# Optimization experiments

Hardware: AMD Instinct MI355X
Metric: run time of the kernel (lower is better)

The kernel has to match this reference:

```python
import jax, jax.numpy as jnp
import numpy as np

N = 40000       # nodes
E = 400000      # directed edges (before self-loops)
F_IN = 50       # PPI num_features
HID = 64        # per-head hidden
H = 4           # heads
NCLS = 121      # PPI num_classes
NEG_SLOPE = 0.2


def gat_layer(x, src, dst, W, a_src, a_dst, W_res, b, concat):
    """PyG GATConv: per-edge attention, segment softmax over dst, scatter-add."""
    n = x.shape[0]
    h, c = a_src.shape
    feat = (x @ W).reshape(n, h, c)                       # [N,H,C]
    al_s = (feat * a_src[None]).sum(-1)                   # [N,H]
    al_d = (feat * a_dst[None]).sum(-1)                   # [N,H]
    e = jax.nn.leaky_relu(al_s[src] + al_d[dst], NEG_SLOPE)  # [E,H]
    m = jax.ops.segment_max(e, dst, num_segments=n)       # stable softmax max
    e = jnp.exp(e - m[dst])
    denom = jax.ops.segment_sum(e, dst, num_segments=n)
    w = e / (denom[dst] + 1e-16)                          # [E,H] attention
    msg = feat[src] * w[:, :, None]                       # [E,H,C]
    out = jax.ops.segment_sum(msg, dst, num_segments=n)   # [N,H,C]
    out = out.reshape(n, h * c) if concat else out.mean(axis=1)
    return out + x @ W_res + b                            # residual proj + bias


def setup_inputs() -> dict:
    key = jax.random.key(0)
    ks = jax.random.split(key, 18)
    g = lambda k, shape: jax.random.normal(k, shape, dtype=jnp.float32) * 0.1
    return {
        "x": jax.random.normal(ks[0], (N, F_IN), dtype=jnp.float32),
        "edge_index": jax.random.randint(ks[1], (2, E), 0, N, dtype=jnp.int32),
        "W1": g(ks[2], (F_IN, H * HID)), "a1s": g(ks[3], (H, HID)), "a1d": g(ks[4], (H, HID)),
        "Wr1": g(ks[5], (F_IN, H * HID)), "b1": jnp.zeros((H * HID,), jnp.float32),
        "W2": g(ks[6], (H * HID, H * HID)), "a2s": g(ks[7], (H, HID)), "a2d": g(ks[8], (H, HID)),
        "Wr2": g(ks[9], (H * HID, H * HID)), "b2": jnp.zeros((H * HID,), jnp.float32),
        "W3": g(ks[10], (H * HID, H * NCLS)), "a3s": g(ks[11], (H, NCLS)), "a3d": g(ks[12], (H, NCLS)),
        "Wr3": g(ks[13], (H * HID, NCLS)), "b3": jnp.zeros((NCLS,), jnp.float32),
    }


def reference(x, edge_index, W1, a1s, a1d, Wr1, b1, W2, a2s, a2d, Wr2, b2,
              W3, a3s, a3d, Wr3, b3):
    loop = jnp.arange(N, dtype=edge_index.dtype)          # add_self_loops=True
    src = jnp.concatenate([edge_index[0], loop])
    dst = jnp.concatenate([edge_index[1], loop])
    h = jax.nn.relu(gat_layer(x, src, dst, W1, a1s, a1d, Wr1, b1, True))
    h = jax.nn.relu(gat_layer(h, src, dst, W2, a2s, a2d, Wr2, b2, True))
    return gat_layer(h, src, dst, W3, a3s, a3d, Wr3, b3, False)
```

## Files before the change

kernel.cpp:

```cpp
#include <hip/hip_runtime.h>
#include <hip/hip_bf16.h>


#define NNODES 40000
#define MPAD   40064
#define NEDGES 400000
#define FIN    50
#define NHEAD  4
#define SCANB  157
#define N4     160000

typedef __attribute__((ext_vector_type(8))) short short8;
typedef __attribute__((ext_vector_type(4))) float float4v;
typedef __attribute__((ext_vector_type(2))) float float2v;
typedef __attribute__((ext_vector_type(4))) unsigned short ushort4v;
typedef __attribute__((ext_vector_type(8))) unsigned short ushort8v;
typedef __attribute__((ext_vector_type(4))) unsigned int uint4v;

__device__ inline unsigned short f2bf(float f) {
    union { float f; unsigned u; } v; v.f = f;
    unsigned r = v.u + 0x7fff + ((v.u >> 16) & 1);
    return (unsigned short)(r >> 16);
}
__device__ inline float bf2f(unsigned short u) {
    union { unsigned u; float f; } v; v.u = ((unsigned)u) << 16; return v.f;
}
__device__ inline float lrelu(float x) { return x >= 0.f ? x : 0.2f * x; }

__global__ void hist_kernel(const int* __restrict__ dst, int* __restrict__ counts, int E) {
    int i = blockIdx.x * blockDim.x + threadIdx.x;
    if (i < E) atomicAdd(&counts[dst[i]], 1);
}

__global__ __launch_bounds__(256) void scan_local(const int* __restrict__ counts,
                                                  int* __restrict__ offsets,
                                                  int* __restrict__ partials) {
    __shared__ int sh[256];
    int b = blockIdx.x, t = threadIdx.x, i = b * 256 + t;
    int v = (i < NNODES) ? counts[i] : 0;
    sh[t] = v;
    __syncthreads();
    #pragma unroll
    for (int off = 1; off < 256; off <<= 1) {
        int u = (t >= off) ? sh[t - off] : 0;
        __syncthreads();
        sh[t] += u;
        __syncthreads();
    }
    if (i < NNODES) offsets[i] = sh[t] - v;
    if (t == 255) partials[b] = sh[255];
}

__global__ __launch_bounds__(256) void scan_partials(int* __restrict__ partials,
                                                     int* __restrict__ pexcl) {
    __shared__ int sh[256];
    int t = threadIdx.x;
    int v = (t < SCANB) ? partials[t] : 0;
    sh[t] = v;
    __syncthreads();
    #pragma unroll
    for (int off = 1; off < 256; off <<= 1) {
        int u = (t >= off) ? sh[t - off] : 0;
        __syncthreads();
        sh[t] += u;
        __syncthreads();
    }
    pexcl[t] = sh[t] - v;
}

__global__ __launch_bounds__(256) void scan_carry(int* __restrict__ offsets,
                                                  const int* __restrict__ pexcl) {
    int b = blockIdx.x, i = b * 256 + threadIdx.x;
    if (i < NNODES) offsets[i] += pexcl[b];
}

__global__ void scatter_kernel(const int* __restrict__ src, const int* __restrict__ dst,
                               int* __restrict__ offsets,
                               int* __restrict__ csr_src, int* __restrict__ csr_dst, int E) {
    int i = blockIdx.x * blockDim.x + threadIdx.x;
    if (i < E) {
        int d = dst[i];
        int pos = atomicAdd(&offsets[d], 1);
        csr_src[pos] = src[i];
        csr_dst[pos] = d;
    }
}

__global__ void edge_p(const float* __restrict__ al4,
                       const int* __restrict__ csr_src, const int* __restrict__ csr_dst,
                       float* __restrict__ p4, int E) {
    int j = blockIdx.x * blockDim.x + threadIdx.x;
    if (j >= E) return;
    int s = csr_src[j], d = csr_dst[j];
    float4v a0 = *(const float4v*)&al4[s * 4];
    float4v a1 = *(const float4v*)&al4[2 * N4 + s * 4];
    float4v b0 = *(const float4v*)&al4[N4 + d * 4];
    float4v b1 = *(const float4v*)&al4[3 * N4 + d * 4];
    float4v p;
    p.x = __expf(lrelu(a0.x + a1.x + b0.x + b1.x));
    p.y = __expf(lrelu(a0.y + a1.y + b0.y + b1.y));
    p.z = __expf(lrelu(a0.z + a1.z + b0.z + b1.z));
    p.w = __expf(lrelu(a0.w + a1.w + b0.w + b1.w));
    *(float4v*)&p4[(size_t)j * 4] = p;
}

__global__ void convert_x(const float* __restrict__ x, short* __restrict__ xb) {
    int i = blockIdx.x * blockDim.x + threadIdx.x;
    if (i >= MPAD * 64) return;
    int r = i >> 6, k = i & 63;
    float v = (r < NNODES && k < FIN) ? x[r * FIN + k] : 0.f;
    xb[i] = f2bf(v);
}

__global__ void convert_pack1(const float* __restrict__ W1, const float* __restrict__ Wr1,
                              const float* __restrict__ W2, const float* __restrict__ Wr2,
                              short* __restrict__ wc1, short* __restrict__ wc2) {
    int i = blockIdx.x * blockDim.x + threadIdx.x;
    if (i < 32768) {
        const float* W = (i < 16384) ? W1 : Wr1;
        int j = i & 16383;
        int n = j >> 6, k = j & 63;
        wc1[i] = f2bf((k < FIN) ? W[k * 256 + n] : 0.f);
    } else if (i < 163840) {
        int j = (i - 32768) & 65535;
        const float* W = (i < 98304) ? W2 : Wr2;
        int n = j >> 8, k = j & 255;
        wc2[(i - 32768)] = f2bf(W[k * 256 + n]);
    }
}

__global__ void convert_pack2(const float* __restrict__ W3, const float* __restrict__ Wr3,
                              const float* __restrict__ a3s, const float* __restrict__ a3d,
                              short* __restrict__ wc3,
                              float* __restrict__ a3sp, float* __restrict__ a3dp) {
    int i = blockIdx.x * blockDim.x + threadIdx.x;
    if (i < 131072) {
        int j = i >> 8, k = i & 255;
        int h = j >> 7, c = j & 127;
        wc3[i] = f2bf((c < 121) ? W3[k * 484 + h * 121 + c] : 0.f);
    } else if (i < 163840) {
        int j = i - 131072;
        int n = j >> 8, k = j & 255;
        wc3[131072 + j] = f2bf((n < 121) ? Wr3[k * 121 + n] : 0.f);
    } else if (i < 164864) {
        int j = i - 163840;
        int which = j >> 9; int jj = j & 511;
        int h = jj >> 7, c = jj & 127;
        float v = (c < 121) ? (which ? a3d[h * 121 + c] : a3s[h * 121 + c]) : 0.f;
        (which ? a3dp : a3sp)[jj] = v;
    }
}

__global__ void convert_f8(const unsigned short* __restrict__ Fb, unsigned int* __restrict__ F8) {
    int i = blockIdx.x * blockDim.x + threadIdx.x;
    if (i >= NNODES * 128) return;
    ushort4v f = *(const ushort4v*)&Fb[(size_t)i * 4];
    int v = 0;
    v = __builtin_amdgcn_cvt_pk_fp8_f32(bf2f(f.x), bf2f(f.y), v, false);
    v = __builtin_amdgcn_cvt_pk_fp8_f32(bf2f(f.z), bf2f(f.w), v, true);
    F8[i] = (unsigned int)v;
}

template<int MODE>
__global__ __launch_bounds__(256) void mfma_gemm_fused(const short* __restrict__ A,
                                                       const short* __restrict__ Bt,
                                                       const float* __restrict__ bias,
                                                       const float* __restrict__ asv,
                                                       const float* __restrict__ adv,
                                                       unsigned short* __restrict__ Fb,
                                                       unsigned short* __restrict__ Rb,
                                                       float* __restrict__ out,
                                                       float* __restrict__ al4,
                                                       int Kp) {
    const int NW = MODE ? 512 : 256;
    __shared__ __align__(16) short As[4096];
    __shared__ __align__(16) unsigned short Cs[2][32][132];
    const int tid = threadIdx.x;
    const int l   = tid & 63;
    const int w   = tid >> 6;
    const int wm  = w >> 1, wn = w & 1;
    const int row0 = blockIdx.y * 128;
    const int col0 = blockIdx.x * 128;
    const int lrow = l & 15;
    const int lq   = l >> 4;
    const int sr = (tid >> 6) * 16 + (tid & 15);
    const int sk = ((tid >> 4) & 3) * 8;

    float4v acc[4][4] = {};

    for (int k0 = 0; k0 < Kp; k0 += 32) {
        short8 a0 = *(const short8*)&A[(size_t)(row0 + sr) * Kp + k0 + sk];
        short8 a1 = *(const short8*)&A[(size_t)(row0 + 64 + sr) * Kp + k0 + sk];
        short8 bfrag[4];
        #pragma unroll
        for (int ct = 0; ct < 4; ++ct) {
            int col = col0 + wn * 64 + ct * 16 + lrow;
            bfrag[ct] = *(const short8*)&Bt[(size_t)col * Kp + k0 + lq * 8];
        }
        __syncthreads();
        *(short8*)&As[tid * 8] = a0;
        *(short8*)&As[(tid + 256) * 8] = a1;
        __syncthreads();
        #pragma unroll
        for (int rt = 0; rt < 4; ++rt) {
            short8 afrag = *(const short8*)&As[(wm * 4 + rt) * 512 + l * 8];
            #pragma unroll
            for (int ct = 0; ct < 4; ++ct)
                acc[rt][ct] = __builtin_amdgcn_mfma_f32_16x16x32_bf16(afrag, bfrag[ct],
                                                                      acc[rt][ct], 0, 0, 0);
        }
    }

    const int colbase = col0 + wn * 64;
    const bool isW = colbase < NW;

    if (isW) {
        const int head = (colbase * NHEAD) / NW;
        const int half = MODE ? ((colbase >> 6) & 1) : 0;
        float* als_o = al4 + (half ? 2 * N4 : 0);
        float* ald_o = als_o + N4;
        float as_c[4], ad_c[4];
        #pragma unroll
        for (int ct = 0; ct < 4; ++ct) {
            int col = colbase + ct * 16 + lrow;
            as_c[ct] = asv[col];
            ad_c[ct] = adv[col];
        }
        #pragma unroll
        for (int rt = 0; rt < 4; ++rt) {
            #pragma unroll
            for (int i = 0; i < 4; ++i) {
                int r = row0 + wm * 64 + rt * 16 + lq * 4 + i;
                float fs = 0.f, fd = 0.f;
                #pragma unroll
                for (int ct = 0; ct < 4; ++ct) {
                    float v = acc[rt][ct][i];
                    fs += v * as_c[ct];
                    fd += v * ad_c[ct];
                }
                #pragma unroll
                for (int o2 = 8; o2; o2 >>= 1) {
                    fs += __shfl_xor(fs, o2, 16);
                    fd += __shfl_xor(fd, o2, 16);
                }
                if (lrow == 0 && r < NNODES) {
                    als_o[r * 4 + head] = fs;
                    ald_o[r * 4 + head] = fd;
                }
            }
        }
    }

    if (MODE == 1 && col0 >= 512) {
        #pragma unroll
        for (int ct = 0; ct < 4; ++ct) {
            int c = colbase + ct * 16 + lrow - 512;
            if (c >= 121) continue;
            float bv = bias[c];
            #pragma unroll
            for (int rt = 0; rt < 4; ++rt) {
                int rbase = row0 + wm * 64 + rt * 16 + lq * 4;
                #pragma unroll
                for (int i = 0; i < 4; ++i) {
                    int r = rbase + i;
                    if (r < NNODES) out[(size_t)r * 121 + c] = acc[rt][ct][i] + bv;
                }
            }
        }
        return;
    }

    const bool isRb = (MODE == 0) && (col0 >= 256);
    unsigned short* dest = isRb ? Rb : Fb;
    const int ldd = MODE ? 512 : 256;
    const int cold = isRb ? col0 - 256 : col0;
    float badd[4] = {0.f, 0.f, 0.f, 0.f};
    if (isRb) {
        #pragma unroll
        for (int ct = 0; ct < 4; ++ct)
            badd[ct] = bias[col0 - 256 + wn * 64 + ct * 16 + lrow];
    }

    const int rp = tid >> 2, g = rp >> 5, rr = rp & 31, q = tid & 3;
    #pragma unroll
    for (int p = 0; p < 2; ++p) {
        if (p) __syncthreads();
        #pragma unroll
        for (int rt2 = 0; rt2 < 2; ++rt2) {
            int rt = p * 2 + rt2;
            #pragma unroll
            for (int ct = 0; ct < 4; ++ct) {
                int cl = wn * 64 + ct * 16 + lrow;
                #pragma unroll
                for (int i = 0; i < 4; ++i) {
                    int lr = rt2 * 16 + lq * 4 + i;
                    Cs[wm][lr][cl] = f2bf(acc[rt][ct][i] + badd[ct]);
                }
            }
        }
        __syncthreads();
        int grow = row0 + g * 64 + p * 32 + rr;
        if (grow < NNODES) {
            #pragma unroll
            for (int k = 0; k < 4; ++k) {
                ushort8v v = *(const ushort8v*)&Cs[g][rr][q * 32 + 8 * k];
                *(ushort8v*)&dest[(size_t)grow * ldd + cold + q * 32 + 8 * k] = v;
            }
        }
    }
}

__global__ __launch_bounds__(256) void attn64_kernel(const unsigned short* __restrict__ featb,
                                                     const float* __restrict__ al4,
                                                     const int* __restrict__ offs,
                                                     const int* __restrict__ csr,
                                                     const float* __restrict__ p4,
                                                     const unsigned short* __restrict__ Rb,
                                                     unsigned short* __restrict__ outb) {
    int n = blockIdx.x * 4 + (threadIdx.x >> 6);
    int l = threadIdx.x & 63;
    int half = l >> 5, li = l & 31;
    int h = li >> 3;
    int beg = n ? offs[n - 1] : 0;
    int end = offs[n];

    float a[8] = {};
    float s = 0.f;
    #pragma unroll 4
    for (int j = beg + half; j < end; j += 2) {
        int sn = csr[j];
        float p = p4[(size_t)j * 4 + h];
        s += p;
        ushort8v f = *(const ushort8v*)&featb[(size_t)sn * 256 + 8 * li];
        #pragma unroll
        for (int i = 0; i < 8; ++i) a[i] += p * bf2f(f[i]);
    }
    s += __shfl_xor(s, 32, 64);
    #pragma unroll
    for (int i = 0; i < 8; ++i) a[i] += __shfl_xor(a[i], 32, 64);

    float lg = al4[n * 4 + h] + al4[2 * N4 + n * 4 + h]
             + al4[N4 + n * 4 + h] + al4[3 * N4 + n * 4 + h];
    float p0 = __expf(lrelu(lg));
    s += p0;
    {
        ushort8v f = *(const ushort8v*)&featb[(size_t)n * 256 + 8 * li];
        #pragma unroll
        for (int i = 0; i < 8; ++i) a[i] += p0 * bf2f(f[i]);
    }
    if (half == 0) {
        float inv = 1.f / s;
        ushort8v r = *(const ushort8v*)&Rb[(size_t)n * 256 + 8 * li];
        ushort8v o;
        #pragma unroll
        for (int i = 0; i < 8; ++i) o[i] = f2bf(fmaxf(bf2f(r[i]) + a[i] * inv, 0.f));
        *(ushort8v*)&outb[(size_t)n * 256 + 8 * li] = o;
    }
}

__global__ __launch_bounds__(256) void attn121_kernel(const unsigned int* __restrict__ F8,
                                                      const float* __restrict__ al4,
                                                      const int* __restrict__ offs,
                                                      const int* __restrict__ csr,
                                                      const float* __restrict__ p4,
                                                      float* __restrict__ out) {
    int n = blockIdx.x * 4 + (threadIdx.x >> 6);
    int l = threadIdx.x & 63;
    int half = l >> 5, li = l & 31;
    int h = li >> 3;
    int beg = n ? offs[n - 1] : 0;
    int end = offs[n];

    float a[16] = {};
    float s = 0.f;
    #pragma unroll 2
    for (int j = beg + half; j < end; j += 2) {
        int sn = csr[j];
        float p = p4[(size_t)j * 4 + h];
        s += p;
        uint4v u = *(const uint4v*)&F8[(size_t)sn * 128 + 4 * li];
        #pragma unroll
        for (int k = 0; k < 4; ++k) {
            float2v lo = __builtin_amdgcn_cvt_pk_f32_fp8(u[k], false);
            float2v hi = __builtin_amdgcn_cvt_pk_f32_fp8(u[k], true);
            a[4 * k + 0] += p * lo.x; a[4 * k + 1] += p * lo.y;
            a[4 * k + 2] += p * hi.x; a[4 * k + 3] += p * hi.y;
        }
    }
    s += __shfl_xor(s, 32, 64);
    #pragma unroll
    for (int i = 0; i < 16; ++i) a[i] += __shfl_xor(a[i], 32, 64);

    float lg = al4[n * 4 + h] + al4[2 * N4 + n * 4 + h]
             + al4[N4 + n * 4 + h] + al4[3 * N4 + n * 4 + h];
    float p0 = __expf(lrelu(lg));
    s += p0;
    {
        uint4v u = *(const uint4v*)&F8[(size_t)n * 128 + 4 * li];
        #pragma unroll
        for (int k = 0; k < 4; ++k) {
            float2v lo = __builtin_amdgcn_cvt_pk_f32_fp8(u[k], false);
            float2v hi = __builtin_amdgcn_cvt_pk_f32_fp8(u[k], true);
            a[4 * k + 0] += p0 * lo.x; a[4 * k + 1] += p0 * lo.y;
            a[4 * k + 2] += p0 * hi.x; a[4 * k + 3] += p0 * hi.y;
        }
    }
    float inv = 0.25f / s;
    #pragma unroll
    for (int i = 0; i < 16; ++i) {
        a[i] *= inv;
        a[i] += __shfl_xor(a[i], 8, 64);
        a[i] += __shfl_xor(a[i], 16, 64);
    }
    if (l < 8) {
        #pragma unroll
        for (int i = 0; i < 16; ++i) {
            int c = 16 * l + i;
            if (c < 121) out[(size_t)n * 121 + c] += a[i];
        }
    }
}

extern "C" void kernel_launch(void* const* d_in, const int* in_sizes, int n_in,
                              void* d_out, int out_size, void* d_ws, size_t ws_size,
                              hipStream_t stream) {
    const float* x   = (const float*)d_in[0];
    const int* ei    = (const int*)d_in[1];
    const float* W1  = (const float*)d_in[2];
    const float* a1s = (const float*)d_in[3];
    const float* a1d = (const float*)d_in[4];
    const float* Wr1 = (const float*)d_in[5];
    const float* b1  = (const float*)d_in[6];
    const float* W2  = (const float*)d_in[7];
    const float* a2s = (const float*)d_in[8];
    const float* a2d = (const float*)d_in[9];
    const float* Wr2 = (const float*)d_in[10];
    const float* b2  = (const float*)d_in[11];
    const float* W3  = (const float*)d_in[12];
    const float* a3s = (const float*)d_in[13];
    const float* a3d = (const float*)d_in[14];
    const float* Wr3 = (const float*)d_in[15];
    const float* b3  = (const float*)d_in[16];
    float* out = (float*)d_out;

    const int* e_src = ei;
    const int* e_dst = ei + NEDGES;

    char* ws = (char*)d_ws;
    size_t off = 0;
    auto carve = [&](size_t bytes) { void* p = ws + off; off += (bytes + 255) & ~255ull; return p; };
    unsigned short* Fb = (unsigned short*)carve((size_t)MPAD * 512 * 2);
    unsigned short* Rb = (unsigned short*)carve((size_t)MPAD * 256 * 2);
    unsigned short* Hb = (unsigned short*)carve((size_t)MPAD * 256 * 2);
    unsigned int* F8 = (unsigned int*)carve((size_t)NNODES * 128 * 4);
    short* xb   = (short*)carve((size_t)MPAD * 64 * 2);
    short* wc1  = (short*)carve((size_t)512 * 64 * 2);
    short* wc2  = (short*)carve((size_t)512 * 256 * 2);
    short* wc3  = (short*)carve((size_t)640 * 256 * 2);
    float* a3sp = (float*)carve(512 * 4);
    float* a3dp = (float*)carve(512 * 4);
    float* al4  = (float*)carve((size_t)4 * N4 * 4);
    float* p4   = (float*)carve((size_t)NEDGES * 4 * 4);
    int* csr_src = (int*)carve((size_t)NEDGES * 4);
    int* csr_dst = (int*)carve((size_t)NEDGES * 4);
    int* offsets = (int*)carve(((size_t)NNODES + 4) * 4);
    int* counts  = (int*)carve((size_t)NNODES * 4);
    int* partials = (int*)carve(256 * 4);
    int* pexcl    = (int*)carve(256 * 4);

    const int EB = (NEDGES + 255) / 256;
    dim3 blk(256);

    convert_x<<<(MPAD * 64 + 255) / 256, blk, 0, stream>>>(x, xb);
    convert_pack1<<<(163840 + 255) / 256, blk, 0, stream>>>(W1, Wr1, W2, Wr2, wc1, wc2);
    convert_pack2<<<(164864 + 255) / 256, blk, 0, stream>>>(W3, Wr3, a3s, a3d, wc3, a3sp, a3dp);

    hipMemsetAsync(al4 + 2 * N4, 0, (size_t)2 * N4 * 4, stream);

    hipMemsetAsync(counts, 0, NNODES * 4, stream);
    hist_kernel<<<EB, blk, 0, stream>>>(e_dst, counts, NEDGES);
    scan_local<<<SCANB, blk, 0, stream>>>(counts, offsets, partials);
    scan_partials<<<1, blk, 0, stream>>>(partials, pexcl);
    scan_carry<<<SCANB, blk, 0, stream>>>(offsets, pexcl);
    scatter_kernel<<<EB, blk, 0, stream>>>(e_src, e_dst, offsets, csr_src, csr_dst, NEDGES);

    mfma_gemm_fused<0><<<dim3(4, 313), blk, 0, stream>>>(xb, wc1, b1, a1s, a1d,
                                                         Fb, Rb, nullptr, al4, 64);
    edge_p<<<EB, blk, 0, stream>>>(al4, csr_src, csr_dst, p4, NEDGES);
    attn64_kernel<<<NNODES / 4, blk, 0, stream>>>(Fb, al4, offsets, csr_src, p4, Rb, Hb);

    mfma_gemm_fused<0><<<dim3(4, 313), blk, 0, stream>>>((short*)Hb, wc2, b2, a2s, a2d,
                                                         Fb, Rb, nullptr, al4, 256);
    edge_p<<<EB, blk, 0, stream>>>(al4, csr_src, csr_dst, p4, NEDGES);
    attn64_kernel<<<NNODES / 4, blk, 0, stream>>>(Fb, al4, offsets, csr_src, p4, Rb, Hb);

    mfma_gemm_fused<1><<<dim3(5, 313), blk, 0, stream>>>((short*)Hb, wc3, b3, a3sp, a3dp,
                                                         Fb, nullptr, out, al4, 256);
    convert_f8<<<(NNODES * 128 + 255) / 256, blk, 0, stream>>>(Fb, F8);
    edge_p<<<EB, blk, 0, stream>>>(al4, csr_src, csr_dst, p4, NEDGES);
    attn121_kernel<<<NNODES / 4, blk, 0, stream>>>(F8, al4, offsets, csr_src, p4, out);
}
```

Before: 458.3 us.

## Stage GEMM tiles via direct global-to-LDS loads with XCD-aware block remap

The fused MFMA GEMM now loads both A and B tiles straight into LDS with global_load_lds, using K-steps of 64 instead of per-lane register loads of B. It also remaps the flat workgroup index so consecutive tiles land on the same XCD for better L2 reuse, and stages the final-layer fp32 output through LDS so row writes coalesce. The aim is to cut redundant global B traffic and uncoalesced stores. In exchange LDS use grows to 32KB for A/B, which may lower occupancy, and the grid dimensions are hardcoded to 313 row blocks.

```diff
diff --git a/kernel.cpp b/kernel.cpp
--- a/kernel.cpp
+++ b/kernel.cpp
@@ -26,6 +26,12 @@
     union { unsigned u; float f; } v; v.u = ((unsigned)u) << 16; return v.f;
 }
 __device__ inline float lrelu(float x) { return x >= 0.f ? x : 0.2f * x; }
+
+typedef __attribute__((address_space(3))) unsigned int lds_u32;
+typedef __attribute__((address_space(1))) const unsigned int glb_u32;
+__device__ __forceinline__ void gl2lds16(const short* g, short* l) {
+    __builtin_amdgcn_global_load_lds((glb_u32*)g, (lds_u32*)l, 16, 0, 0);
+}
 
 __global__ void hist_kernel(const int* __restrict__ dst, int* __restrict__ counts, int E) {
     int i = blockIdx.x * blockDim.x + threadIdx.x;
@@ -172,42 +178,59 @@
                                                        float* __restrict__ out,
                                                        float* __restrict__ al4,
                                                        int Kp) {
-    const int NW = MODE ? 512 : 256;
-    __shared__ __align__(16) short As[4096];
+    const int NW  = MODE ? 512 : 256;
+    const int NCB = MODE ? 5 : 4;
+    __shared__ __align__(16) short AsBs[16384];
     __shared__ __align__(16) unsigned short Cs[2][32][132];
+    short* As = AsBs;
+    short* Bs = AsBs + 8192;
+
     const int tid = threadIdx.x;
     const int l   = tid & 63;
     const int w   = tid >> 6;
     const int wm  = w >> 1, wn = w & 1;
-    const int row0 = blockIdx.y * 128;
-    const int col0 = blockIdx.x * 128;
     const int lrow = l & 15;
     const int lq   = l >> 4;
-    const int sr = (tid >> 6) * 16 + (tid & 15);
-    const int sk = ((tid >> 4) & 3) * 8;
+
+    const int T = NCB * 313;
+    const int flat = blockIdx.y * NCB + blockIdx.x;
+    const int q8 = T >> 3, r8 = T & 7;
+    const int xcd = flat & 7, sidx = flat >> 3;
+    const int wg = (xcd < r8 ? xcd * (q8 + 1) : r8 * (q8 + 1) + (xcd - r8) * q8) + sidx;
+    const int row0 = (wg / NCB) * 128;
+    const int col0 = (wg % NCB) * 128;
 
     float4v acc[4][4] = {};
 
-    for (int k0 = 0; k0 < Kp; k0 += 32) {
-        short8 a0 = *(const short8*)&A[(size_t)(row0 + sr) * Kp + k0 + sk];
-        short8 a1 = *(const short8*)&A[(size_t)(row0 + 64 + sr) * Kp + k0 + sk];
-        short8 bfrag[4];
-        #pragma unroll
-        for (int ct = 0; ct < 4; ++ct) {
-            int col = col0 + wn * 64 + ct * 16 + lrow;
-            bfrag[ct] = *(const short8*)&Bt[(size_t)col * Kp + k0 + lq * 8];
+    const int lr_ld = tid >> 3;
+    const int lk_ld = (tid & 7) * 8;
+    const int nk = Kp >> 6;
+    for (int t = 0; t < nk; ++t) {
+        const int k0 = t << 6;
+        if (t) __syncthreads();
+        const size_t abase = (size_t)(row0 + lr_ld) * Kp + k0 + lk_ld;
+        const size_t bbase = (size_t)(col0 + lr_ld) * Kp + k0 + lk_ld;
+        #pragma unroll
+        for (int j = 0; j < 4; ++j) {
+            gl2lds16(&A[abase + (size_t)j * 32 * Kp],  &As[j * 2048 + tid * 8]);
+            gl2lds16(&Bt[bbase + (size_t)j * 32 * Kp], &Bs[j * 2048 + tid * 8]);
         }
         __syncthreads();
-        *(short8*)&As[tid * 8] = a0;
-        *(short8*)&As[(tid + 256) * 8] = a1;
-        __syncthreads();
-        #pragma unroll
-        for (int rt = 0; rt < 4; ++rt) {
-            short8 afrag = *(const short8*)&As[(wm * 4 + rt) * 512 + l * 8];
+        #pragma unroll
+        for (int ks = 0; ks < 2; ++ks) {
+            short8 aF[4], bF[4];
+            #pragma unroll
+            for (int rt = 0; rt < 4; ++rt)
+                aF[rt] = *(const short8*)&As[(wm * 64 + rt * 16 + lrow) * 64 + ks * 32 + lq * 8];
             #pragma unroll
             for (int ct = 0; ct < 4; ++ct)
-                acc[rt][ct] = __builtin_amdgcn_mfma_f32_16x16x32_bf16(afrag, bfrag[ct],
-                                                                      acc[rt][ct], 0, 0, 0);
+                bF[ct] = *(const short8*)&Bs[(wn * 64 + ct * 16 + lrow) * 64 + ks * 32 + lq * 8];
+            #pragma unroll
+            for (int rt = 0; rt < 4; ++rt)
+                #pragma unroll
+                for (int ct = 0; ct < 4; ++ct)
+                    acc[rt][ct] = __builtin_amdgcn_mfma_f32_16x16x32_bf16(aF[rt], bF[ct],
+                                                                          acc[rt][ct], 0, 0, 0);
         }
     }
 
@@ -252,19 +275,34 @@
     }
 
     if (MODE == 1 && col0 >= 512) {
-        #pragma unroll
-        for (int ct = 0; ct < 4; ++ct) {
-            int c = colbase + ct * 16 + lrow - 512;
-            if (c >= 121) continue;
-            float bv = bias[c];
-            #pragma unroll
-            for (int rt = 0; rt < 4; ++rt) {
-                int rbase = row0 + wm * 64 + rt * 16 + lq * 4;
+        float* Ls = (float*)AsBs;
+        #pragma unroll
+        for (int p = 0; p < 4; ++p) {
+            __syncthreads();
+            if (wm == (p >> 1)) {
+                const int rt0 = (p & 1) * 2;
                 #pragma unroll
-                for (int i = 0; i < 4; ++i) {
-                    int r = rbase + i;
-                    if (r < NNODES) out[(size_t)r * 121 + c] = acc[rt][ct][i] + bv;
+                for (int rt2 = 0; rt2 < 2; ++rt2) {
+                    int rt = rt0 + rt2;
+                    #pragma unroll
+                    for (int ct = 0; ct < 4; ++ct) {
+                        int cl = wn * 64 + ct * 16 + lrow;
+                        #pragma unroll
+                        for (int i = 0; i < 4; ++i) {
+                            int lr = rt2 * 16 + lq * 4 + i;
+                            Ls[lr * 132 + cl] = acc[rt][ct][i];
+                        }
+                    }
                 }
+            }
+            __syncthreads();
+            #pragma unroll
+            for (int it = 0; it < 16; ++it) {
+                int idx = it * 256 + tid;
+                int r = idx >> 7, c = idx & 127;
+                int grow = row0 + p * 32 + r;
+                if (c < 121 && grow < NNODES)
+                    out[(size_t)grow * 121 + c] = Ls[r * 132 + c] + bias[c];
             }
         }
         return;
@@ -281,7 +319,7 @@
             badd[ct] = bias[col0 - 256 + wn * 64 + ct * 16 + lrow];
     }
 
-    const int rp = tid >> 2, g = rp >> 5, rr = rp & 31, q = tid & 3;
+    const int rp = tid >> 2, g = rp >> 5, rr = rp & 31, qq = tid & 3;
     #pragma unroll
     for (int p = 0; p < 2; ++p) {
         if (p) __syncthreads();
@@ -303,8 +341,8 @@
         if (grow < NNODES) {
             #pragma unroll
             for (int k = 0; k < 4; ++k) {
-                ushort8v v = *(const ushort8v*)&Cs[g][rr][q * 32 + 8 * k];
-                *(ushort8v*)&dest[(size_t)grow * ldd + cold + q * 32 + 8 * k] = v;
+                ushort8v v = *(const ushort8v*)&Cs[g][rr][qq * 32 + 8 * k];
+                *(ushort8v*)&dest[(size_t)grow * ldd + cold + qq * 32 + 8 * k] = v;
             }
         }
     }
```

Result: faster. 427.1 us (-6.8%).
